# Performance work log

Measured on AMD Instinct MI355X. Metric: run time of the kernel, lower is better.

The kernel has to match this reference:

```python
import jax, jax.numpy as jnp
import numpy as np

T = 4096          # num tokens
HID = 2048        # hidden_size
HQ = 32           # num q heads
HKV = 8           # num kv heads
G = HQ // HKV     # GQA group size
D = 128           # head_dim (q/k)
DV = 96           # v_head_dim
W = 512           # sliding window (= query block size)
THETA = 1e6
Q_SIZE, K_SIZE, V_SIZE = HQ * D, HKV * D, HKV * DV


def setup_inputs() -> dict:
    key = jax.random.key(0)
    k1, k2, k3, k4 = jax.random.split(key, 4)
    positions = jnp.arange(T, dtype=jnp.int32)
    hidden_states = jax.random.normal(k1, (T, HID), dtype=jnp.float32)
    qkv_w = jax.random.normal(k2, (Q_SIZE + K_SIZE + V_SIZE, HID), dtype=jnp.float32) * (HID ** -0.5)
    o_w = jax.random.normal(k3, (HID, HQ * DV), dtype=jnp.float32) * ((HQ * DV) ** -0.5)
    sink_bias = jax.random.normal(k4, (HQ,), dtype=jnp.float32)
    return {"positions": positions, "hidden_states": hidden_states,
            "qkv_w": qkv_w, "o_w": o_w, "sink_bias": sink_bias}


def _rope(x, positions):
    # neox-style rotate-half RoPE on full head_dim (partial_rotary_factor=1.0)
    half = D // 2
    inv_freq = 1.0 / (THETA ** (jnp.arange(0, half, dtype=jnp.float32) / half))
    ang = positions.astype(jnp.float32)[:, None] * inv_freq[None, :]   # [T, D/2]
    cos = jnp.cos(ang)[:, None, :]
    sin = jnp.sin(ang)[:, None, :]
    x1, x2 = x[..., :half], x[..., half:]
    return jnp.concatenate([x1 * cos - x2 * sin, x2 * cos + x1 * sin], axis=-1)


def _swa_with_sink(q, k, v, sink_bias):
    # q: [T, HKV, G, D], k: [T, HKV, D], v: [T, HKV, DV]
    nb = T // W
    scale = D ** -0.5
    qb = q.reshape(nb, W, HKV, G, D)
    # per query block i, keys/values from global span [(i-1)*W, (i+1)*W)
    k_pad = jnp.pad(k, ((W, 0), (0, 0), (0, 0)))
    v_pad = jnp.pad(v, ((W, 0), (0, 0), (0, 0)))
    idx = jnp.arange(nb)[:, None] * W + jnp.arange(2 * W)[None, :]     # [nb, 2W]
    k_ext = k_pad[idx]                                                 # [nb, 2W, HKV, D]
    v_ext = v_pad[idx]                                                 # [nb, 2W, HKV, DV]
    # mask: rel = t - j in [0, W); exclude left-pad keys (key_pos < 0)
    r = jnp.arange(W)[:, None]
    c = jnp.arange(2 * W)[None, :]
    rel = W + r - c                                                    # [W, 2W]
    key_pos = (jnp.arange(nb)[:, None, None] - 1) * W + c[None]        # [nb, W(1), 2W]
    mask = (rel >= 0) & (rel < W) & (key_pos >= 0)                     # [nb, W, 2W]
    scores = jnp.einsum('nrkgd,nckd->nkgrc', qb, k_ext) * scale        # [nb,HKV,G,W,2W]
    scores = jnp.where(mask[:, None, None, :, :], scores, -jnp.inf)
    sink = jnp.broadcast_to(sink_bias.reshape(HKV, G)[None, :, :, None, None],
                            (nb, HKV, G, W, 1))
    logits = jnp.concatenate([scores, sink], axis=-1)                  # [...,2W+1]
    p = jax.nn.softmax(logits, axis=-1)[..., :-1]                      # drop sink column
    out = jnp.einsum('nkgrc,nckd->nrkgd', p, v_ext)                    # [nb,W,HKV,G,DV]
    return out.reshape(T, HQ * DV)


def reference(positions, hidden_states, qkv_w, o_w, sink_bias):
    qkv = hidden_states @ qkv_w.T                                      # [T, Q+K+V]
    q, k, v = jnp.split(qkv, [Q_SIZE, Q_SIZE + K_SIZE], axis=-1)
    q = q.reshape(T, HQ, D)
    k = k.reshape(T, HKV, D)
    v = v.reshape(T, HKV, DV)
    q = _rope(q, positions).reshape(T, HKV, G, D)
    k = _rope(k, positions)
    attn = _swa_with_sink(q, k, v, sink_bias)                          # [T, HQ*DV]
    return attn @ o_w.T                                                # [T, HID]
```

## Files before the change

kernel.cpp:

```cpp
#include <hip/hip_runtime.h>
#include <hip/hip_bf16.h>
#include <stdint.h>

#define T_SEQ 4096
#define HIDDEN 2048
#define NQH 32
#define NKVH 8
#define DH 128
#define DVH 96
#define WWIN 512
#define QKVN 5888
#define KOFF 4096
#define VOFF 5120
#define ATTN 3072
#define QSCALE 0.08838834764831845f

typedef uint16_t u16;
typedef uint32_t u32;
typedef __bf16 bfrag8 __attribute__((ext_vector_type(8)));
typedef float f32x4v __attribute__((ext_vector_type(4)));
typedef float f32x16 __attribute__((ext_vector_type(16)));

__device__ __forceinline__ u16 f2bf(float x) {
  u32 u = __float_as_uint(x);
  return (u16)((u + 0x7fffu + ((u >> 16) & 1u)) >> 16);
}
__device__ __forceinline__ float bf2f(u16 v) { return __uint_as_float(((u32)v) << 16); }

__device__ __forceinline__ void gload16(const u16* src, char* ldst) {
  __builtin_amdgcn_global_load_lds((const __attribute__((address_space(1))) u32*)src,
                                   (__attribute__((address_space(3))) u32*)ldst, 16, 0, 0);
}

__global__ void cvt_kernel(const float* __restrict__ in, u16* __restrict__ out, int n4) {
  int i = blockIdx.x * blockDim.x + threadIdx.x;
  int st = gridDim.x * blockDim.x;
  for (; i < n4; i += st) {
    float4 v = ((const float4*)in)[i];
    ushort4 o;
    o.x = f2bf(v.x); o.y = f2bf(v.y); o.z = f2bf(v.z); o.w = f2bf(v.w);
    ((ushort4*)out)[i] = o;
  }
}

template<int OUT_F32>
__global__ __launch_bounds__(512, 2) void gemm_v3(const u16* __restrict__ A,
                                                  const u16* __restrict__ B,
                                                  void* __restrict__ Cp,
                                                  int M, int N, int K, int nbm) {
  extern __shared__ char lds[];
  const int tid = threadIdx.x;
  const int w = tid >> 6, lane = tid & 63;
  const int wr = w >> 1, wc = w & 1;
  const int r5 = lane & 31, kg = lane >> 5;

  const int nwg = gridDim.x;
  int bid = (int)blockIdx.x;
  if ((nwg & 7) == 0) bid = (bid & 7) * (nwg >> 3) + (bid >> 3);
  const int bm = (bid % nbm) * 256;
  const int bn = (bid / nbm) * 128;
  const int NT = K >> 6;

  f32x16 acc[2][2];
#pragma unroll
  for (int mb = 0; mb < 2; mb++)
#pragma unroll
    for (int nb = 0; nb < 2; nb++)
#pragma unroll
      for (int i = 0; i < 16; i++) acc[mb][nb][i] = 0.f;

  const int q = r5 * 128 + ((kg ^ (r5 & 7)) << 4);

  auto stageA = [&](int t) {
    char* dst = lds + (t % 3) * 49152;
    const u16* Abase = A + (size_t)bm * K + ((size_t)t << 6);
#pragma unroll
    for (int i = 0; i < 4; i++) {
      int D = (w * 4 + i) * 1024 + lane * 16;
      int row = D >> 7;
      int kb = (D ^ ((row & 7) << 4)) & 127;
      gload16(Abase + (size_t)row * K + (kb >> 1), dst + D);
    }
  };
  auto stageB = [&](int t) {
    char* dst = lds + (t % 3) * 49152 + 32768;
    const u16* Bbase = B + (size_t)bn * K + ((size_t)t << 6);
#pragma unroll
    for (int i = 0; i < 2; i++) {
      int D = (w * 2 + i) * 1024 + lane * 16;
      int row = D >> 7;
      int kb = (D ^ ((row & 7) << 4)) & 127;
      gload16(Bbase + (size_t)row * K + (kb >> 1), dst + D);
    }
  };

  stageA(0); stageB(0);

  for (int t = 0; t < NT; ++t) {
    const char* Ab = lds + (t % 3) * 49152 + wr * 8192;
    const char* Bb = lds + (t % 3) * 49152 + 32768 + wc * 8192;
    if (t + 1 < NT) {
      stageA(t + 1);
      stageB(t + 1);
      asm volatile("s_waitcnt vmcnt(6)");
    } else {
      asm volatile("s_waitcnt vmcnt(0)");
    }
    asm volatile("s_barrier" ::: "memory");

    bfrag8 af[2][2], bf[2][2];
#pragma unroll
    for (int ks = 0; ks < 2; ks++) {
#pragma unroll
      for (int mb = 0; mb < 2; mb++)
        af[mb][ks] = *(const bfrag8*)(Ab + mb * 4096 + (q ^ (ks << 5)));
#pragma unroll
      for (int nb = 0; nb < 2; nb++)
        bf[nb][ks] = *(const bfrag8*)(Bb + nb * 4096 + (q ^ (ks << 5)));
    }
    __builtin_amdgcn_s_setprio(1);
#pragma unroll
    for (int ks = 0; ks < 2; ks++)
#pragma unroll
      for (int mb = 0; mb < 2; mb++)
#pragma unroll
        for (int nb = 0; nb < 2; nb++)
          acc[mb][nb] = __builtin_amdgcn_mfma_f32_32x32x16_bf16(af[mb][ks], bf[nb][ks], acc[mb][nb], 0, 0, 0);
    __builtin_amdgcn_s_setprio(0);

    bfrag8 af2[2][2], bf2[2][2];
#pragma unroll
    for (int ks = 0; ks < 2; ks++) {
#pragma unroll
      for (int mb = 0; mb < 2; mb++)
        af2[mb][ks] = *(const bfrag8*)(Ab + mb * 4096 + (q ^ ((ks + 2) << 5)));
#pragma unroll
      for (int nb = 0; nb < 2; nb++)
        bf2[nb][ks] = *(const bfrag8*)(Bb + nb * 4096 + (q ^ ((ks + 2) << 5)));
    }
    __builtin_amdgcn_s_setprio(1);
#pragma unroll
    for (int ks = 0; ks < 2; ks++)
#pragma unroll
      for (int mb = 0; mb < 2; mb++)
#pragma unroll
        for (int nb = 0; nb < 2; nb++)
          acc[mb][nb] = __builtin_amdgcn_mfma_f32_32x32x16_bf16(af2[mb][ks], bf2[nb][ks], acc[mb][nb], 0, 0, 0);
    __builtin_amdgcn_s_setprio(0);
  }

  const int rb0 = bm + wr * 64;
  const int cb0 = bn + wc * 64;
#pragma unroll
  for (int mb = 0; mb < 2; mb++)
#pragma unroll
    for (int nb = 0; nb < 2; nb++)
#pragma unroll
      for (int i = 0; i < 16; i++) {
        int rowl = (i & 3) + 8 * (i >> 2) + 4 * kg;
        size_t off = (size_t)(rb0 + mb * 32 + rowl) * N + cb0 + nb * 32 + r5;
        if (OUT_F32) ((float*)Cp)[off] = acc[mb][nb][i];
        else         ((u16*)Cp)[off] = f2bf(acc[mb][nb][i]);
      }
}

template<int OUT_F32>
__global__ __launch_bounds__(256) void gemm_nt(const u16* __restrict__ A,
                                               const u16* __restrict__ B,
                                               void* __restrict__ Cp,
                                               int M, int N, int K) {
  __shared__ u16 Asm[128 * 32];
  __shared__ u16 Bsm[128 * 32];
  const int tid = threadIdx.x;
  const int wv = tid >> 6, lane = tid & 63;
  const int bm = blockIdx.x * 128, bn = blockIdx.y * 128;
  const int wm = (wv >> 1) * 64, wn = (wv & 1) * 64;
  const int srow = lane >> 2;
  const int scol = (lane & 3) * 8;
  const int fr = lane & 15, fk = (lane >> 4) * 8;
  f32x4v acc[4][4];
#pragma unroll
  for (int i = 0; i < 4; i++)
#pragma unroll
    for (int j = 0; j < 4; j++) acc[i][j] = {0.f, 0.f, 0.f, 0.f};

  for (int kt = 0; kt < K; kt += 32) {
    __syncthreads();
#pragma unroll
    for (int c = 0; c < 2; c++) {
      const int ci = wv * 2 + c;
      const u16* ga = A + (size_t)(bm + ci * 16 + srow) * K + kt + scol;
      const u16* gb = B + (size_t)(bn + ci * 16 + srow) * K + kt + scol;
      gload16(ga, (char*)(Asm + ci * 512));
      gload16(gb, (char*)(Bsm + ci * 512));
    }
    __syncthreads();
    bfrag8 af[4], bf[4];
#pragma unroll
    for (int i = 0; i < 4; i++) af[i] = *(const bfrag8*)(Asm + (wm + i * 16 + fr) * 32 + fk);
#pragma unroll
    for (int j = 0; j < 4; j++) bf[j] = *(const bfrag8*)(Bsm + (wn + j * 16 + fr) * 32 + fk);
#pragma unroll
    for (int i = 0; i < 4; i++)
#pragma unroll
      for (int j = 0; j < 4; j++)
        acc[i][j] = __builtin_amdgcn_mfma_f32_16x16x32_bf16(af[i], bf[j], acc[i][j], 0, 0, 0);
  }
  const int orow = (lane >> 4) * 4, ocol = lane & 15;
#pragma unroll
  for (int i = 0; i < 4; i++)
#pragma unroll
    for (int j = 0; j < 4; j++) {
      size_t base = (size_t)(bm + wm + i * 16 + orow) * N + (size_t)(bn + wn + j * 16 + ocol);
#pragma unroll
      for (int r = 0; r < 4; r++) {
        if (OUT_F32) ((float*)Cp)[base + (size_t)r * N] = acc[i][j][r];
        else         ((u16*)Cp)[base + (size_t)r * N] = f2bf(acc[i][j][r]);
      }
    }
}

__global__ void rope_kernel(u16* __restrict__ qkv, const int* __restrict__ pos) {
  int gid = blockIdx.x * 256 + threadIdx.x;
  int d = gid & 63;
  int r = gid >> 6;
  int hh = r % 40;
  int t = r / 40;
  if (t >= T_SEQ) return;
  int off = (hh < 32) ? hh * 128 : KOFF + (hh - 32) * 128;
  u16* p = qkv + (size_t)t * QKVN + off + d;
  float x1 = bf2f(p[0]);
  float x2 = bf2f(p[64]);
  float inv_freq = exp2f(-(float)d * 0.3114307588956852f);
  float ang = (float)pos[t] * inv_freq;
  float c = cosf(ang), s = sinf(ang);
  float y1 = x1 * c - x2 * s;
  float y2 = x2 * c + x1 * s;
  if (hh < 32) { y1 *= QSCALE; y2 *= QSCALE; }
  p[0] = f2bf(y1);
  p[64] = f2bf(y2);
}

__global__ __launch_bounds__(256) void vt_kernel(const u16* __restrict__ qkv,
                                                 u16* __restrict__ vt) {
  __shared__ u16 tile[64][100];
  const int t0 = blockIdx.x * 64;
  const int hk = blockIdx.y;
  const int tid = threadIdx.x;
#pragma unroll
  for (int i = 0; i < 3; i++) {
    int idx = i * 256 + tid;
    int row = idx / 12, ch = idx % 12;
    const u16* g = qkv + (size_t)(t0 + row) * QKVN + VOFF + hk * DVH + ch * 8;
    uint2 a = *(const uint2*)g;
    uint2 b = *(const uint2*)(g + 4);
    *(uint2*)&tile[row][ch * 8] = a;
    *(uint2*)&tile[row][ch * 8 + 4] = b;
  }
  __syncthreads();
#pragma unroll
  for (int i = 0; i < 3; i++) {
    int idx = i * 256 + tid;
    int dv = idx >> 3, tc = (idx & 7) * 8;
    union { uint4 v4; u16 s[8]; } o;
#pragma unroll
    for (int j = 0; j < 8; j++) o.s[j] = tile[tc + j][dv];
    *(uint4*)(vt + (((size_t)(hk * 96 + dv)) << 12) + t0 + tc) = o.v4;
  }
}

__global__ __launch_bounds__(256, 2) void attn_mfma(const u16* __restrict__ qkv,
                                                    const u16* __restrict__ vt,
                                                    const float* __restrict__ sink_bias,
                                                    u16* __restrict__ attn_out) {
  extern __shared__ char smem[];

  const int tid = threadIdx.x;
  const int wv = tid >> 6;
  const int lane = tid & 63;
  const int g = lane >> 4;
  const int c = lane & 15;
  const int t0 = blockIdx.x * 32;
  const int hk = blockIdx.y;
  const int h = hk * 4 + wv;
  u16* pw = (u16*)(smem + 57344 + wv * 4096);

  bfrag8 qf[2][4];
#pragma unroll
  for (int m = 0; m < 2; m++)
#pragma unroll
    for (int kf = 0; kf < 4; kf++)
      qf[m][kf] = *(const bfrag8*)(qkv + (size_t)(t0 + m * 16 + c) * QKVN + h * DH + kf * 32 + g * 8);

  f32x4v acc_o[2][6];
#pragma unroll
  for (int m = 0; m < 2; m++)
#pragma unroll
    for (int n = 0; n < 6; n++) acc_o[m][n] = {0.f, 0.f, 0.f, 0.f};

  const float sb = sink_bias[h];
  float m_run[2][4], l_run[2][4];
#pragma unroll
  for (int m = 0; m < 2; m++)
#pragma unroll
    for (int r = 0; r < 4; r++) { m_run[m][r] = sb; l_run[m][r] = 1.0f; }

  int cb0 = t0 - (WWIN - 1);
  cb0 = (cb0 < 0) ? 0 : (cb0 & ~63);
  const int nc = (t0 + 32 - cb0 + 63) >> 6;

  auto stage = [&](int ci) {
    const int cb = cb0 + ci * 64;
    char* kd = smem + (ci & 1) * 16384;
    char* vd = smem + 32768 + (ci & 1) * 12288;
#pragma unroll
    for (int it = 0; it < 4; it++) {
      int dest = it * 4096 + tid * 16;
      int row = dest >> 8;
      int src = dest ^ ((row & 7) << 4);
      gload16(qkv + (size_t)(cb + row) * QKVN + KOFF + hk * DH + ((src & 255) >> 1), kd + dest);
    }
#pragma unroll
    for (int it = 0; it < 3; it++) {
      int dest = it * 4096 + tid * 16;
      int row = dest >> 7;
      int src = dest ^ ((row & 7) << 4);
      gload16(vt + (((size_t)(hk * 96 + row)) << 12) + cb + ((src & 127) >> 1), vd + dest);
    }
  };

  stage(0);
  if (nc > 1) stage(1);

  for (int ci = 0; ci < nc; ci++) {
    const int cb = cb0 + ci * 64;
    const char* k_lds = smem + (ci & 1) * 16384;
    const char* v_lds = smem + 32768 + (ci & 1) * 12288;
    if (ci + 1 < nc) asm volatile("s_waitcnt vmcnt(7)");
    else             asm volatile("s_waitcnt vmcnt(0)");
    asm volatile("s_barrier" ::: "memory");

    f32x4v s[2][4];
#pragma unroll
    for (int m = 0; m < 2; m++)
#pragma unroll
      for (int n = 0; n < 4; n++) s[m][n] = {0.f, 0.f, 0.f, 0.f};
#pragma unroll
    for (int kf = 0; kf < 4; kf++) {
      bfrag8 kb[4];
#pragma unroll
      for (int n = 0; n < 4; n++) {
        int key = n * 16 + c;
        int byt = ((key << 8) + (kf << 6) + (g << 4)) ^ ((key & 7) << 4);
        kb[n] = *(const bfrag8*)(k_lds + byt);
      }
#pragma unroll
      for (int m = 0; m < 2; m++)
#pragma unroll
        for (int n = 0; n < 4; n++)
          s[m][n] = __builtin_amdgcn_mfma_f32_16x16x32_bf16(qf[m][kf], kb[n], s[m][n], 0, 0, 0);
    }

    if ((cb + 63 > t0) || (cb + WWIN < t0 + 32)) {
#pragma unroll
      for (int m = 0; m < 2; m++)
#pragma unroll
        for (int n = 0; n < 4; n++)
#pragma unroll
          for (int r = 0; r < 4; r++) {
            int rel = (t0 + m * 16 + g * 4 + r) - (cb + n * 16 + c);
            if (!(rel >= 0 && rel < WWIN)) s[m][n][r] = -3.0e38f;
          }
    }

    float corr[2][4];
#pragma unroll
    for (int m = 0; m < 2; m++)
#pragma unroll
      for (int r = 0; r < 4; r++) {
        float v0 = fmaxf(fmaxf(s[m][0][r], s[m][1][r]), fmaxf(s[m][2][r], s[m][3][r]));
        v0 = fmaxf(v0, __shfl_xor(v0, 1));
        v0 = fmaxf(v0, __shfl_xor(v0, 2));
        v0 = fmaxf(v0, __shfl_xor(v0, 4));
        v0 = fmaxf(v0, __shfl_xor(v0, 8));
        float mn = fmaxf(m_run[m][r], v0);
        corr[m][r] = __expf(m_run[m][r] - mn);
        m_run[m][r] = mn;
        float p0 = __expf(s[m][0][r] - mn);
        float p1 = __expf(s[m][1][r] - mn);
        float p2 = __expf(s[m][2][r] - mn);
        float p3 = __expf(s[m][3][r] - mn);
        s[m][0][r] = p0; s[m][1][r] = p1; s[m][2][r] = p2; s[m][3][r] = p3;
        float rs = p0 + p1 + p2 + p3;
        rs += __shfl_xor(rs, 1);
        rs += __shfl_xor(rs, 2);
        rs += __shfl_xor(rs, 4);
        rs += __shfl_xor(rs, 8);
        l_run[m][r] = l_run[m][r] * corr[m][r] + rs;
      }
#pragma unroll
    for (int m = 0; m < 2; m++)
#pragma unroll
      for (int n = 0; n < 6; n++)
#pragma unroll
      for (int r = 0; r < 4; r++) acc_o[m][n][r] *= corr[m][r];

#pragma unroll
    for (int m = 0; m < 2; m++)
#pragma unroll
      for (int n = 0; n < 4; n++) {
        u32 lo = (u32)f2bf(s[m][n][0]) | ((u32)f2bf(s[m][n][1]) << 16);
        u32 hi = (u32)f2bf(s[m][n][2]) | ((u32)f2bf(s[m][n][3]) << 16);
        int byt = ((m * 2 + (n >> 1)) << 10) | (g << 3) | ((c & 3) << 5) |
                  (((c >> 2) & 1) << 9) | ((((n & 1) * 2) + (c >> 3)) << 7);
        uint2 u; u.x = lo; u.y = hi;
        *(uint2*)((char*)pw + byt) = u;
      }

#pragma unroll
    for (int ks = 0; ks < 2; ks++) {
      bfrag8 pa[2];
#pragma unroll
      for (int m = 0; m < 2; m++) {
        union { bfrag8 v; u16 s16[8]; } u;
#pragma unroll
        for (int j = 0; j < 4; j++) {
          int e = ((m * 2 + ks) << 9) + c + j * 16 + g * 64;
          u.s16[j] = pw[e];
          u.s16[4 + j] = pw[e + 256];
        }
        pa[m] = u.v;
      }
#pragma unroll
      for (int n = 0; n < 6; n++) {
        int dv = n * 16 + c;
        int byt = ((dv << 7) + (ks << 6) + (g << 4)) ^ ((dv & 7) << 4);
        bfrag8 vb = *(const bfrag8*)(v_lds + byt);
#pragma unroll
        for (int m = 0; m < 2; m++)
          acc_o[m][n] = __builtin_amdgcn_mfma_f32_16x16x32_bf16(pa[m], vb, acc_o[m][n], 0, 0, 0);
      }
    }

    asm volatile("s_barrier" ::: "memory");
    if (ci + 2 < nc) stage(ci + 2);
  }

#pragma unroll
  for (int m = 0; m < 2; m++) {
    float inv[4];
#pragma unroll
    for (int r = 0; r < 4; r++) inv[r] = 1.0f / l_run[m][r];
#pragma unroll
    for (int n = 0; n < 6; n++)
#pragma unroll
      for (int r = 0; r < 4; r++) {
        int tq = t0 + m * 16 + g * 4 + r;
        attn_out[(size_t)tq * ATTN + h * DVH + n * 16 + c] = f2bf(acc_o[m][n][r] * inv[r]);
      }
  }
}

extern "C" void kernel_launch(void* const* d_in, const int* in_sizes, int n_in,
                              void* d_out, int out_size, void* d_ws, size_t ws_size,
                              hipStream_t stream) {
  const int* positions = (const int*)d_in[0];
  const float* hidden = (const float*)d_in[1];
  const float* qkv_w = (const float*)d_in[2];
  const float* o_w = (const float*)d_in[3];
  const float* sink = (const float*)d_in[4];
  char* ws = (char*)d_ws;

  u16* hs_bf   = (u16*)(ws + 0);
  u16* w1_bf   = (u16*)(ws + 16777216);
  u16* attn_bf = (u16*)(ws + 0);
  u16* vt_buf  = (u16*)(ws + 25165824);
  u16* w2_bf   = (u16*)(ws + 40894464);
  u16* qkv_bf  = (u16*)(ws + 53477376);

  bool v3Ok =
    (hipFuncSetAttribute((const void*)&gemm_v3<0>,
                         hipFuncAttributeMaxDynamicSharedMemorySize, 147456) == hipSuccess) &&
    (hipFuncSetAttribute((const void*)&gemm_v3<1>,
                         hipFuncAttributeMaxDynamicSharedMemorySize, 147456) == hipSuccess);
  bool atOk = (hipFuncSetAttribute((const void*)&attn_mfma,
                 hipFuncAttributeMaxDynamicSharedMemorySize, 73728) == hipSuccess);
  (void)atOk;

  cvt_kernel<<<dim3(1024), dim3(256), 0, stream>>>(hidden, hs_bf, 8388608 / 4);
  cvt_kernel<<<dim3(1024), dim3(256), 0, stream>>>(qkv_w, w1_bf, 12058624 / 4);
  cvt_kernel<<<dim3(1024), dim3(256), 0, stream>>>(o_w, w2_bf, 6291456 / 4);

  if (v3Ok)
    gemm_v3<0><<<dim3(736), dim3(512), 147456, stream>>>(hs_bf, w1_bf, (void*)qkv_bf,
                                                         T_SEQ, QKVN, HIDDEN, 16);
  else
    gemm_nt<0><<<dim3(32, 46), dim3(256), 0, stream>>>(hs_bf, w1_bf, (void*)qkv_bf,
                                                       T_SEQ, QKVN, HIDDEN);

  rope_kernel<<<dim3(40960), dim3(256), 0, stream>>>(qkv_bf, positions);
  vt_kernel<<<dim3(T_SEQ / 64, NKVH), dim3(256), 0, stream>>>(qkv_bf, vt_buf);
  attn_mfma<<<dim3(T_SEQ / 32, NKVH), dim3(256), 73728, stream>>>(qkv_bf, vt_buf, sink, attn_bf);

  if (v3Ok)
    gemm_v3<1><<<dim3(256), dim3(512), 147456, stream>>>(attn_bf, w2_bf, d_out,
                                                         T_SEQ, HIDDEN, ATTN, 16);
  else
    gemm_nt<1><<<dim3(32, 16), dim3(256), 0, stream>>>(attn_bf, w2_bf, d_out,
                                                       T_SEQ, HIDDEN, ATTN);
}
```

Before: 313.5 us.

## Add 256x256-tile MFMA GEMM kernel for the QKV projection

Adds a new bf16 GEMM kernel, gemm_v4, that uses 256x256 output tiles, 16x16x32 MFMA instructions, a 2x4 wave layout, XOR-swizzled LDS, and double-buffered direct-to-LDS loads. The QKV projection now uses it instead of the 256x128-tile gemm_v3, halving the grid to 368 workgroups. The goal is more operand reuse per LDS load and fewer global loads per FLOP. In exchange, each thread holds more accumulator registers and the smaller grid can fill the CUs less evenly.

```diff
diff --git a/kernel.cpp b/kernel.cpp
--- a/kernel.cpp
+++ b/kernel.cpp
@@ -41,6 +41,140 @@
     o.x = f2bf(v.x); o.y = f2bf(v.y); o.z = f2bf(v.z); o.w = f2bf(v.w);
     ((ushort4*)out)[i] = o;
   }
+}
+
+__global__ __launch_bounds__(512, 2) void gemm_v4(const u16* __restrict__ A,
+                                                  const u16* __restrict__ Bmat,
+                                                  u16* __restrict__ C,
+                                                  int M, int N, int K, int nbm) {
+  extern __shared__ char lds[];
+  const int tid = threadIdx.x;
+  const int w = tid >> 6, lane = tid & 63;
+  const int wr = w >> 2, wc = w & 3;
+  const int fr = lane & 15, kg = lane >> 4;
+
+  const int nwg = gridDim.x;
+  int bid = (int)blockIdx.x;
+  if ((nwg & 7) == 0) bid = (bid & 7) * (nwg >> 3) + (bid >> 3);
+  const int bm = (bid % nbm) * 256;
+  const int bn = (bid / nbm) * 256;
+  const int NT = K >> 6;
+
+  f32x4v acc[8][4];
+#pragma unroll
+  for (int m = 0; m < 8; m++)
+#pragma unroll
+    for (int n = 0; n < 4; n++) acc[m][n] = {0.f, 0.f, 0.f, 0.f};
+
+  auto stage = [&](int t) {
+    char* dst = lds + (t & 1) * 65536;
+    const u16* Abase = A + (size_t)bm * K + ((size_t)t << 6);
+    const u16* Bbase = Bmat + (size_t)bn * K + ((size_t)t << 6);
+#pragma unroll
+    for (int i = 0; i < 4; i++) {
+      int D = (i * 512 + tid) * 16;
+      int row = D >> 7;
+      int kb = (D ^ ((row & 7) << 4)) & 127;
+      gload16(Abase + (size_t)row * K + (kb >> 1), dst + D);
+    }
+#pragma unroll
+    for (int i = 0; i < 4; i++) {
+      int D = (i * 512 + tid) * 16;
+      int row = D >> 7;
+      int kb = (D ^ ((row & 7) << 4)) & 127;
+      gload16(Bbase + (size_t)row * K + (kb >> 1), dst + 32768 + D);
+    }
+  };
+
+  stage(0);
+  stage(1);
+
+  const int sxor = (fr & 7) << 4;
+
+  for (int t = 0; t < NT; ++t) {
+    const char* Ab = lds + (t & 1) * 65536 + wr * 16384;
+    const char* Bb = lds + (t & 1) * 65536 + 32768 + wc * 8192;
+    if (t + 1 < NT) asm volatile("s_waitcnt vmcnt(8)");
+    else            asm volatile("s_waitcnt vmcnt(0)");
+    asm volatile("s_barrier" ::: "memory");
+
+    bfrag8 afr[4][2], bfr0[2][2], bfr1[2][2];
+
+#pragma unroll
+    for (int mf = 0; mf < 4; mf++)
+#pragma unroll
+      for (int ks = 0; ks < 2; ks++)
+        afr[mf][ks] = *(const bfrag8*)(Ab + (mf * 16 + fr) * 128 + (((ks << 6) | (kg << 4)) ^ sxor));
+#pragma unroll
+    for (int nf = 0; nf < 2; nf++)
+#pragma unroll
+      for (int ks = 0; ks < 2; ks++)
+        bfr0[nf][ks] = *(const bfrag8*)(Bb + (nf * 16 + fr) * 128 + (((ks << 6) | (kg << 4)) ^ sxor));
+    __builtin_amdgcn_s_setprio(1);
+#pragma unroll
+    for (int mf = 0; mf < 4; mf++)
+#pragma unroll
+      for (int nf = 0; nf < 2; nf++)
+#pragma unroll
+        for (int ks = 0; ks < 2; ks++)
+          acc[mf][nf] = __builtin_amdgcn_mfma_f32_16x16x32_bf16(afr[mf][ks], bfr0[nf][ks], acc[mf][nf], 0, 0, 0);
+    __builtin_amdgcn_s_setprio(0);
+
+#pragma unroll
+    for (int nf = 0; nf < 2; nf++)
+#pragma unroll
+      for (int ks = 0; ks < 2; ks++)
+        bfr1[nf][ks] = *(const bfrag8*)(Bb + (32 + nf * 16 + fr) * 128 + (((ks << 6) | (kg << 4)) ^ sxor));
+    __builtin_amdgcn_s_setprio(1);
+#pragma unroll
+    for (int mf = 0; mf < 4; mf++)
+#pragma unroll
+      for (int nf = 0; nf < 2; nf++)
+#pragma unroll
+        for (int ks = 0; ks < 2; ks++)
+          acc[mf][2 + nf] = __builtin_amdgcn_mfma_f32_16x16x32_bf16(afr[mf][ks], bfr1[nf][ks], acc[mf][2 + nf], 0, 0, 0);
+    __builtin_amdgcn_s_setprio(0);
+
+#pragma unroll
+    for (int mf = 0; mf < 4; mf++)
+#pragma unroll
+      for (int ks = 0; ks < 2; ks++)
+        afr[mf][ks] = *(const bfrag8*)(Ab + (64 + mf * 16 + fr) * 128 + (((ks << 6) | (kg << 4)) ^ sxor));
+    __builtin_amdgcn_s_setprio(1);
+#pragma unroll
+    for (int mf = 0; mf < 4; mf++)
+#pragma unroll
+      for (int nf = 0; nf < 2; nf++)
+#pragma unroll
+        for (int ks = 0; ks < 2; ks++)
+          acc[4 + mf][nf] = __builtin_amdgcn_mfma_f32_16x16x32_bf16(afr[mf][ks], bfr0[nf][ks], acc[4 + mf][nf], 0, 0, 0);
+    __builtin_amdgcn_s_setprio(0);
+
+    __builtin_amdgcn_s_setprio(1);
+#pragma unroll
+    for (int mf = 0; mf < 4; mf++)
+#pragma unroll
+      for (int nf = 0; nf < 2; nf++)
+#pragma unroll
+        for (int ks = 0; ks < 2; ks++)
+          acc[4 + mf][2 + nf] = __builtin_amdgcn_mfma_f32_16x16x32_bf16(afr[mf][ks], bfr1[nf][ks], acc[4 + mf][2 + nf], 0, 0, 0);
+    __builtin_amdgcn_s_setprio(0);
+
+    asm volatile("s_barrier" ::: "memory");
+    if (t + 2 < NT) stage(t + 2);
+  }
+
+  const int rb0 = bm + wr * 128;
+  const int cb0 = bn + wc * 64;
+#pragma unroll
+  for (int m = 0; m < 8; m++)
+#pragma unroll
+    for (int n = 0; n < 4; n++) {
+      size_t base = (size_t)(rb0 + m * 16 + kg * 4) * N + cb0 + n * 16 + fr;
+#pragma unroll
+      for (int r = 0; r < 4; r++)
+        C[base + (size_t)r * N] = f2bf(acc[m][n][r]);
+    }
 }
 
 template<int OUT_F32>
@@ -478,22 +612,20 @@
   u16* w2_bf   = (u16*)(ws + 40894464);
   u16* qkv_bf  = (u16*)(ws + 53477376);
 
-  bool v3Ok =
-    (hipFuncSetAttribute((const void*)&gemm_v3<0>,
-                         hipFuncAttributeMaxDynamicSharedMemorySize, 147456) == hipSuccess) &&
-    (hipFuncSetAttribute((const void*)&gemm_v3<1>,
-                         hipFuncAttributeMaxDynamicSharedMemorySize, 147456) == hipSuccess);
-  bool atOk = (hipFuncSetAttribute((const void*)&attn_mfma,
-                 hipFuncAttributeMaxDynamicSharedMemorySize, 73728) == hipSuccess);
-  (void)atOk;
+  bool v4Ok = (hipFuncSetAttribute((const void*)&gemm_v4,
+                 hipFuncAttributeMaxDynamicSharedMemorySize, 131072) == hipSuccess);
+  bool v3Ok = (hipFuncSetAttribute((const void*)&gemm_v3<1>,
+                 hipFuncAttributeMaxDynamicSharedMemorySize, 147456) == hipSuccess);
+  (void)hipFuncSetAttribute((const void*)&attn_mfma,
+                            hipFuncAttributeMaxDynamicSharedMemorySize, 73728);
 
   cvt_kernel<<<dim3(1024), dim3(256), 0, stream>>>(hidden, hs_bf, 8388608 / 4);
   cvt_kernel<<<dim3(1024), dim3(256), 0, stream>>>(qkv_w, w1_bf, 12058624 / 4);
   cvt_kernel<<<dim3(1024), dim3(256), 0, stream>>>(o_w, w2_bf, 6291456 / 4);
 
-  if (v3Ok)
-    gemm_v3<0><<<dim3(736), dim3(512), 147456, stream>>>(hs_bf, w1_bf, (void*)qkv_bf,
-                                                         T_SEQ, QKVN, HIDDEN, 16);
+  if (v4Ok)
+    gemm_v4<<<dim3(368), dim3(512), 131072, stream>>>(hs_bf, w1_bf, qkv_bf,
+                                                      T_SEQ, QKVN, HIDDEN, 16);
   else
     gemm_nt<0><<<dim3(32, 46), dim3(256), 0, stream>>>(hs_bf, w1_bf, (void*)qkv_bf,
                                                        T_SEQ, QKVN, HIDDEN);
```

Measured after the change: 319.1 us. No clear change (+1.8%).
